# Optimization experiments

Measured on AMD Instinct MI355X. Metric: run time of the kernel, lower is better.

Reference implementation:

```python
import jax, jax.numpy as jnp
import numpy as np

SEQ = 4096
D = 1024      # input_dim
DK = 1024     # query_dim
DV = 1024     # encoding_dim
STD = 0.02


def setup_inputs() -> dict:
    key = jax.random.key(0)
    kz, kq, kk, kv = jax.random.split(key, 4)
    z = jax.random.normal(kz, (SEQ, D), dtype=jnp.float32)
    # weights stored as [in, out], matching q = z @ Wq
    Wq = STD * jax.random.normal(kq, (D, DK), dtype=jnp.float32)
    Wk = STD * jax.random.normal(kk, (D, DK), dtype=jnp.float32)
    Wv = STD * jax.random.normal(kv, (D, DV), dtype=jnp.float32)
    return {"z": z, "Wq": Wq, "Wk": Wk, "Wv": Wv}


def reference(z, Wq, Wk, Wv):
    q = z @ Wq                      # [S, dk]
    k = z @ Wk                      # [S, dk]
    v = z @ Wv                      # [S, dv]
    # NOTE: original applies the 1/sqrt(dk) scale AFTER softmax (to the probabilities)
    attn = jax.nn.softmax(q @ k.T, axis=-1) * (DK ** -0.5)  # [S, S]
    return attn @ v                 # [S, dv]
```

## Files before the change

### kernel.cpp

```cpp
#include <hip/hip_runtime.h>

typedef unsigned short u16;
typedef unsigned int u32;
typedef __attribute__((ext_vector_type(8))) short bf16x8;
typedef __attribute__((ext_vector_type(8))) _Float16 f16x8;
typedef __attribute__((ext_vector_type(4))) float f32x4;

__device__ inline u16 f2bf(float f){
  union { float f; unsigned u; } v; v.f = f;
  unsigned r = v.u + 0x7FFFu + ((v.u >> 16) & 1u);
  return (u16)(r >> 16);
}
__device__ inline float bf2f(u16 u){
  union { unsigned u; float f; } v; v.u = ((unsigned)u) << 16;
  return v.f;
}
__device__ inline u16 f2h(float f){
  union { _Float16 h; u16 u; } v; v.h = (_Float16)f; return v.u;
}

__device__ inline void gload16(const u16* g, u16* l){
  __builtin_amdgcn_global_load_lds(
      (const __attribute__((address_space(1))) u32*)(const void*)g,
      (__attribute__((address_space(3))) u32*)(void*)l, 16, 0, 0);
}

#define WAITV(n) asm volatile("s_waitcnt vmcnt(" #n ")" ::: "memory")
#define FENCE()  asm volatile("" ::: "memory")

__global__ __launch_bounds__(256) void split_f32(const float* __restrict__ x,
                                                 u16* __restrict__ hi,
                                                 u16* __restrict__ lo, int n4){
  int i = blockIdx.x * 256 + threadIdx.x;
  if (i >= n4) return;
  float4 v = ((const float4*)x)[i];
  float a0 = v.x, a1 = v.y, a2 = v.z, a3 = v.w;
  u16 h0 = f2bf(a0), h1 = f2bf(a1), h2 = f2bf(a2), h3 = f2bf(a3);
  ushort4 h; h.x = h0; h.y = h1; h.z = h2; h.w = h3;
  ushort4 l; l.x = f2bf(a0 - bf2f(h0)); l.y = f2bf(a1 - bf2f(h1));
  l.z = f2bf(a2 - bf2f(h2)); l.w = f2bf(a3 - bf2f(h3));
  ((ushort4*)hi)[i] = h;
  ((ushort4*)lo)[i] = l;
}

__global__ __launch_bounds__(256) void conv_h16(const float* __restrict__ x,
                                                u16* __restrict__ h16, int n4){
  int i = blockIdx.x * 256 + threadIdx.x;
  if (i >= n4) return;
  float4 v = ((const float4*)x)[i];
  ushort4 g; g.x = f2h(v.x); g.y = f2h(v.y); g.z = f2h(v.z); g.w = f2h(v.w);
  ((ushort4*)h16)[i] = g;
}

__global__ __launch_bounds__(256) void transpose_wv16(
    const float* __restrict__ W, u16* __restrict__ H){
  __shared__ float t[64][65];
  int d0 = blockIdx.y * 64, n0 = blockIdx.x * 64;
  int tid = threadIdx.x;
  int r = tid >> 4, c4 = (tid & 15) * 4;
  for (int rr = r; rr < 64; rr += 16){
    float4 v = *(const float4*)&W[(size_t)(d0 + rr) * 1024 + n0 + c4];
    t[rr][c4 + 0] = v.x; t[rr][c4 + 1] = v.y; t[rr][c4 + 2] = v.z; t[rr][c4 + 3] = v.w;
  }
  __syncthreads();
  int n = tid >> 4, d4 = (tid & 15) * 4;
  for (int nn = n; nn < 64; nn += 16){
    ushort4 h;
    h.x = f2h(t[d4 + 0][nn]); h.y = f2h(t[d4 + 1][nn]);
    h.z = f2h(t[d4 + 2][nn]); h.w = f2h(t[d4 + 3][nn]);
    *(ushort4*)&H[(size_t)(n0 + nn) * 1024 + d0 + d4] = h;
  }
}

template<int IN, int EPI>
__global__ __launch_bounds__(256) void gemm_bt(
    const u16* __restrict__ Ah, const u16* __restrict__ Al, int lda,
    const u16* __restrict__ Bh, const u16* __restrict__ Bl, int ldb,
    void* __restrict__ C0, int ldc, int K, size_t zslab){
  constexpr int NPL = (IN == 0) ? 4 : 2;
  constexpr int DEPTH = (IN == 0) ? 1 : 2;
  constexpr int NBUF = DEPTH + 1;
  __shared__ __align__(16) u16 sm[NBUF * NPL * 4096];

  const int kz = blockIdx.z * K;
  Ah += kz; Bh += kz;
  if constexpr (IN == 0){ Al += kz; Bl += kz; }

  const int tid = threadIdx.x;
  const int lane = tid & 63, wave = tid >> 6;
  const int wr = wave >> 1, wc = wave & 1;
  const int lr = lane & 15, kg = lane >> 4;

  const int nwg = gridDim.x * gridDim.y;
  const int id = blockIdx.y * gridDim.x + blockIdx.x;
  const int chunk = nwg >> 3;
  const int swz = (id & 7) * chunk + (id >> 3);
  const int bx = swz % gridDim.x, by = swz / gridDim.x;
  const int m0 = by * 128, n0 = bx * 128;

  const int l_r = lane >> 2, l_c = lane & 3;
  const int st_chunk = l_c ^ ((l_r + (l_r >> 2)) & 3);
  const int rd_swz = (lr + (lr >> 2)) & 3;

  f32x4 acc[4][4];
  #pragma unroll
  for (int m = 0; m < 4; m++)
    #pragma unroll
    for (int n = 0; n < 4; n++)
      acc[m][n] = (f32x4){0.f, 0.f, 0.f, 0.f};

  auto STAGE = [&](int buf, int k0){
    #pragma unroll
    for (int c = 0; c < NPL * 2; ++c){
      int pc = c * 4 + wave;
      int p = pc >> 3, ch = pc & 7;
      const u16* g; int ld, rb;
      if (IN == 0){
        g = (p == 0) ? Ah : (p == 1) ? Al : (p == 2) ? Bh : Bl;
        ld = (p < 2) ? lda : ldb;  rb = (p < 2) ? m0 : n0;
      } else {
        g = (p == 0) ? Ah : Bh;
        ld = (p == 0) ? lda : ldb; rb = (p == 0) ? m0 : n0;
      }
      int r = ch * 16 + l_r;
      const u16* src = g + (size_t)(rb + r) * ld + k0 + st_chunk * 8;
      u16* dst = &sm[((size_t)buf * NPL + p) * 4096 + ch * 512];
      gload16(src, dst);
    }
  };

  const int KT = K >> 5;
  STAGE(0, 0);
  if constexpr (DEPTH == 2){ if (KT > 1) STAGE(1, 32); }

  int bufc = 0, pfb = DEPTH % NBUF;
  for (int kt = 0; kt < KT; ++kt){
    const int pf = kt + DEPTH;
    if (pf < KT){
      STAGE(pfb, pf * 32);
      WAITV(8);
    } else if (kt + 1 < KT){
      if constexpr (IN == 0) WAITV(8); else WAITV(4);
    } else {
      WAITV(0);
    }
    __builtin_amdgcn_s_barrier();
    FENCE();

    const u16* pA  = &sm[((size_t)bufc * NPL + 0) * 4096];
    const u16* pAl = &sm[((size_t)bufc * NPL + 1) * 4096];
    const u16* pB  = &sm[((size_t)bufc * NPL + (IN == 0 ? 2 : 1)) * 4096];
    const u16* pBl = &sm[((size_t)bufc * NPL + 3) * 4096];

    const int slot = (kg ^ rd_swz) * 8;
    bf16x8 afh[4], bfh[4], afl[4], bfl[4];
    f16x8 ah16[4], bh16[4];
    #pragma unroll
    for (int m = 0; m < 4; m++){
      int r = wr * 64 + m * 16 + lr;
      if (IN == 2) ah16[m] = *(const f16x8*)&pA[r * 32 + slot];
      else {
        afh[m] = *(const bf16x8*)&pA[r * 32 + slot];
        if (IN == 0) afl[m] = *(const bf16x8*)&pAl[r * 32 + slot];
      }
    }
    #pragma unroll
    for (int n = 0; n < 4; n++){
      int r = wc * 64 + n * 16 + lr;
      if (IN == 2) bh16[n] = *(const f16x8*)&pB[r * 32 + slot];
      else {
        bfh[n] = *(const bf16x8*)&pB[r * 32 + slot];
        if (IN == 0) bfl[n] = *(const bf16x8*)&pBl[r * 32 + slot];
      }
    }
    #pragma unroll
    for (int m = 0; m < 4; m++)
      #pragma unroll
      for (int n = 0; n < 4; n++){
        if (IN == 2){
          acc[m][n] = __builtin_amdgcn_mfma_f32_16x16x32_f16(ah16[m], bh16[n], acc[m][n], 0, 0, 0);
        } else {
          acc[m][n] = __builtin_amdgcn_mfma_f32_16x16x32_bf16(afh[m], bfh[n], acc[m][n], 0, 0, 0);
          if (IN == 0){
            acc[m][n] = __builtin_amdgcn_mfma_f32_16x16x32_bf16(afl[m], bfh[n], acc[m][n], 0, 0, 0);
            acc[m][n] = __builtin_amdgcn_mfma_f32_16x16x32_bf16(afh[m], bfl[n], acc[m][n], 0, 0, 0);
          }
        }
      }
    FENCE();
    __builtin_amdgcn_s_barrier();
    bufc = (bufc + 1 == NBUF) ? 0 : bufc + 1;
    pfb  = (pfb  + 1 == NBUF) ? 0 : pfb  + 1;
  }

  const int row0 = m0 + wr * 64, col0 = n0 + wc * 64 + lr;
  #pragma unroll
  for (int m = 0; m < 4; m++)
    #pragma unroll
    for (int n = 0; n < 4; n++)
      #pragma unroll
      for (int r = 0; r < 4; r++){
        int row = row0 + m * 16 + kg * 4 + r;
        int col = col0 + n * 16;
        float x = acc[m][n][r];
        if (EPI == 0){
          float* C = (float*)C0 + (size_t)blockIdx.z * zslab;
          C[(size_t)row * ldc + col] = x;
        } else {
          ((u16*)C0)[(size_t)row * ldc + col] = f2h(x);
        }
      }
}

__global__ __launch_bounds__(512, 1) void gemm256(
    const u16* __restrict__ A, int lda,
    const u16* __restrict__ B, int ldb,
    float* __restrict__ C0z, int l0, float* __restrict__ C1z, int l1,
    float* __restrict__ C2z, int l2, float* __restrict__ C3z, int l3,
    int K){
  __shared__ __align__(16) u16 sm[2 * 32768];

  const int tid = threadIdx.x;
  const int lane = tid & 63, wave = tid >> 6;
  const int wr = wave >> 2, wc = wave & 3;
  const int lr = lane & 15, kg = lane >> 4;
  const int g7 = lr & 7;

  const int nwg = gridDim.x * gridDim.y;
  const int id = blockIdx.y * gridDim.x + blockIdx.x;
  const int chunk = nwg >> 3;
  const int swz = (id & 7) * chunk + (id >> 3);
  const int bx = swz % gridDim.x, by = swz / gridDim.x;
  const int m0 = by * 256, n0 = bx * 256;

  A += (size_t)blockIdx.z * (size_t)K;
  B += (size_t)blockIdx.z * (size_t)K;
  float* Cp; int ldc;
  if (blockIdx.z == 0){ Cp = C0z; ldc = l0; }
  else if (blockIdx.z == 1){ Cp = C1z; ldc = l1; }
  else if (blockIdx.z == 2){ Cp = C2z; ldc = l2; }
  else { Cp = C3z; ldc = l3; }

  auto STAGE = [&](int buf, int k0){
    #pragma unroll
    for (int rd = 0; rd < 8; ++rd){
      int p = rd >> 2;
      int r0 = (rd & 3) * 64 + wave * 8;
      const u16* g = p ? B : A;
      int ld = p ? ldb : lda;
      int rb = p ? n0 : m0;
      int grow = rb + r0 + (lane >> 3);
      int gch = (lane & 7) ^ (lane >> 3);
      const u16* src = g + (size_t)grow * ld + k0 + gch * 8;
      u16* dst = &sm[(size_t)buf * 32768 + p * 16384 + r0 * 64];
      gload16(src, dst);
    }
  };

  f32x4 acc[8][4];
  #pragma unroll
  for (int m = 0; m < 8; m++)
    #pragma unroll
    for (int n = 0; n < 4; n++)
      acc[m][n] = (f32x4){0.f, 0.f, 0.f, 0.f};

  const int KT = K >> 6;
  STAGE(0, 0);

  int bufc = 0;
  for (int kt = 0; kt < KT; ++kt){
    WAITV(0);
    __builtin_amdgcn_s_barrier();
    FENCE();
    if (kt + 1 < KT) STAGE(bufc ^ 1, (kt + 1) * 64);

    const u16* pA = &sm[(size_t)bufc * 32768];
    const u16* pB = pA + 16384;
    #pragma unroll
    for (int ks = 0; ks < 2; ++ks){
      f16x8 b[4], a[8];
      #pragma unroll
      for (int n = 0; n < 4; n++){
        int R = wc * 64 + n * 16 + lr;
        b[n] = *(const f16x8*)&pB[R * 64 + (((ks * 4 + kg) ^ g7) * 8)];
      }
      #pragma unroll
      for (int m = 0; m < 8; m++){
        int R = wr * 128 + m * 16 + lr;
        a[m] = *(const f16x8*)&pA[R * 64 + (((ks * 4 + kg) ^ g7) * 8)];
      }
      __builtin_amdgcn_s_setprio(1);
      #pragma unroll
      for (int m = 0; m < 8; m++)
        #pragma unroll
        for (int n = 0; n < 4; n++)
          acc[m][n] = __builtin_amdgcn_mfma_f32_16x16x32_f16(a[m], b[n], acc[m][n], 0, 0, 0);
      __builtin_amdgcn_s_setprio(0);
    }
    FENCE();
    bufc ^= 1;
  }

  const int row0 = m0 + wr * 128, col0 = n0 + wc * 64 + lr;
  #pragma unroll
  for (int m = 0; m < 8; m++)
    #pragma unroll
    for (int n = 0; n < 4; n++)
      #pragma unroll
      for (int r = 0; r < 4; r++){
        int row = row0 + m * 16 + kg * 4 + r;
        int col = col0 + n * 16;
        Cp[(size_t)row * ldc + col] = acc[m][n][r];
      }
}

__global__ __launch_bounds__(256) void reduce_t(u16* __restrict__ dst,
                                                const float* __restrict__ s0,
                                                const float* __restrict__ s1,
                                                const float* __restrict__ s2,
                                                const float* __restrict__ s3){
  int idx = blockIdx.x * 256 + threadIdx.x;
  float4 a = ((const float4*)s0)[idx];
  float4 b = ((const float4*)s1)[idx];
  float4 c = ((const float4*)s2)[idx];
  float4 d = ((const float4*)s3)[idx];
  ushort4 o;
  o.x = f2h((a.x + b.x) + (c.x + d.x));
  o.y = f2h((a.y + b.y) + (c.y + d.y));
  o.z = f2h((a.z + b.z) + (c.z + d.z));
  o.w = f2h((a.w + b.w) + (c.w + d.w));
  ((ushort4*)dst)[idx] = o;
}

__global__ __launch_bounds__(256) void reduce_pv(float* __restrict__ out,
                                                 const float* __restrict__ Sf,
                                                 const float* __restrict__ s3){
  int idx = blockIdx.x * 256 + threadIdx.x;
  int r = idx >> 8, c4 = (idx & 255) * 4;
  float4 a = ((const float4*)out)[idx];
  float4 b = ((const float4*)s3)[idx];
  float4 h1 = *(const float4*)&Sf[(size_t)r * 4096 + 2048 + c4];
  float4 h2 = *(const float4*)&Sf[(size_t)r * 4096 + 3072 + c4];
  float4 o;
  o.x = (a.x + b.x) + (h1.x + h2.x);
  o.y = (a.y + b.y) + (h1.y + h2.y);
  o.z = (a.z + b.z) + (h1.z + h2.z);
  o.w = (a.w + b.w) + (h1.w + h2.w);
  ((float4*)out)[idx] = o;
}

__global__ __launch_bounds__(256) void softmax_rows(float* __restrict__ S){
  int rrow = blockIdx.x;
  float* srow = S + (size_t)rrow * 4096;
  __shared__ float e[4096];
  __shared__ float red[4];
  int tid = threadIdx.x;

  float m = -1e30f;
  for (int i = tid * 4; i < 4096; i += 1024){
    float4 v = *(const float4*)(srow + i);
    m = fmaxf(m, fmaxf(fmaxf(v.x, v.y), fmaxf(v.z, v.w)));
  }
  for (int o = 32; o > 0; o >>= 1) m = fmaxf(m, __shfl_xor(m, o));
  if ((tid & 63) == 0) red[tid >> 6] = m;
  __syncthreads();
  m = fmaxf(fmaxf(red[0], red[1]), fmaxf(red[2], red[3]));

  float s = 0.f;
  for (int i = tid * 4; i < 4096; i += 1024){
    float4 v = *(const float4*)(srow + i);
    float4 ev;
    ev.x = __expf(v.x - m); ev.y = __expf(v.y - m);
    ev.z = __expf(v.z - m); ev.w = __expf(v.w - m);
    s += (ev.x + ev.y) + (ev.z + ev.w);
    *(float4*)&e[i] = ev;
  }
  for (int o = 32; o > 0; o >>= 1) s += __shfl_xor(s, o);
  __syncthreads();
  if ((tid & 63) == 0) red[tid >> 6] = s;
  __syncthreads();
  s = (red[0] + red[1]) + (red[2] + red[3]);

  float scale = 0.03125f / s;
  u16* prow = (u16*)((char*)S + (size_t)rrow * 16384);
  for (int i = tid * 4; i < 4096; i += 1024){
    float4 v = *(const float4*)&e[i];
    ushort4 o; o.x = f2h(v.x * scale); o.y = f2h(v.y * scale);
    o.z = f2h(v.z * scale); o.w = f2h(v.w * scale);
    *(ushort4*)(prow + i) = o;
  }
}

extern "C" void kernel_launch(void* const* d_in, const int* in_sizes, int n_in,
                              void* d_out, int out_size, void* d_ws, size_t ws_size,
                              hipStream_t stream){
  const float* z  = (const float*)d_in[0];
  const float* Wq = (const float*)d_in[1];
  const float* Wk = (const float*)d_in[2];
  const float* Wv = (const float*)d_in[3];
  char* ws = (char*)d_ws;
  const size_t MB = 1ull << 20;

  u16* t16   = (u16*)(ws + 0 * MB);
  u16* z16   = (u16*)(ws + 8 * MB);
  u16* vt16  = (u16*)(ws + 16 * MB);
  float* S   = (float*)(ws + 24 * MB);
  u16* m16   = (u16*)(ws + 88 * MB);
  float* slab3 = (float*)(ws + 0 * MB);
  u16* wqh   = (u16*)(ws + 24 * MB);
  u16* wql   = (u16*)(ws + 26 * MB);
  u16* wkh   = (u16*)(ws + 28 * MB);
  u16* wkl   = (u16*)(ws + 30 * MB);
  u16* wvt16 = (u16*)(ws + 32 * MB);
  float* msl = (float*)(ws + 40 * MB);

  conv_h16<<<4096, 256, 0, stream>>>(z, z16, 4096 * 1024 / 4);
  split_f32<<<1024, 256, 0, stream>>>(Wq, wqh, wql, 1024 * 1024 / 4);
  split_f32<<<1024, 256, 0, stream>>>(Wk, wkh, wkl, 1024 * 1024 / 4);
  transpose_wv16<<<dim3(16, 16), 256, 0, stream>>>(Wv, wvt16);

  gemm_bt<0, 0><<<dim3(8, 8, 4), 256, 0, stream>>>(wkh, wkl, 1024,
      wqh, wql, 1024, msl, 1024, 256, (size_t)1024 * 1024);
  reduce_t<<<1024, 256, 0, stream>>>(m16, msl, msl + 1048576,
      msl + 2097152, msl + 3145728);

  gemm_bt<2, 1><<<dim3(32, 8), 256, 0, stream>>>(wvt16, nullptr, 1024,
      z16, nullptr, 1024, vt16, 4096, 1024, 0);

  gemm_bt<2, 1><<<dim3(8, 32), 256, 0, stream>>>(z16, nullptr, 1024,
      m16, nullptr, 1024, t16, 1024, 1024, 0);

  gemm256<<<dim3(16, 16, 1), 512, 0, stream>>>(t16, 1024, z16, 1024,
      S, 4096, S, 4096, S, 4096, S, 4096, 1024);

  softmax_rows<<<4096, 256, 0, stream>>>(S);

  gemm256<<<dim3(4, 16, 4), 512, 0, stream>>>((u16*)S, 8192, vt16, 4096,
      (float*)d_out, 1024, S + 2048, 4096, S + 3072, 4096, slab3, 1024, 1024);

  reduce_pv<<<4096, 256, 0, stream>>>((float*)d_out, S, slab3);
}
```

Before: 176.2 us.

## Store scores in fp16, merge projection GEMMs and split kernels into single launches

The QK^T score matrix is now written as fp16 instead of fp32, which halves the score write and the softmax read traffic, and softmax works in place on fp16. The two f16 projection GEMMs (V^T and T = z·M) are merged into one 512-block launch, and the Wq/Wk split kernels are merged into one, to cut launch count and tail effects. The split-K partials of P·V now go to dedicated slabs. Rounding the logits to fp16 before softmax adds precision risk on the scores.

```diff
diff --git a/kernel.cpp b/kernel.cpp
--- a/kernel.cpp
+++ b/kernel.cpp
@@ -28,11 +28,15 @@
 #define WAITV(n) asm volatile("s_waitcnt vmcnt(" #n ")" ::: "memory")
 #define FENCE()  asm volatile("" ::: "memory")
 
-__global__ __launch_bounds__(256) void split_f32(const float* __restrict__ x,
-                                                 u16* __restrict__ hi,
-                                                 u16* __restrict__ lo, int n4){
-  int i = blockIdx.x * 256 + threadIdx.x;
-  if (i >= n4) return;
+__global__ __launch_bounds__(256) void split_wqk(const float* __restrict__ wq,
+                                                 const float* __restrict__ wk,
+                                                 u16* __restrict__ qh, u16* __restrict__ ql,
+                                                 u16* __restrict__ kh, u16* __restrict__ kl){
+  int b = blockIdx.x;
+  const float* x; u16 *hi, *lo;
+  int i;
+  if (b < 1024){ x = wq; hi = qh; lo = ql; i = b * 256 + threadIdx.x; }
+  else         { x = wk; hi = kh; lo = kl; i = (b - 1024) * 256 + threadIdx.x; }
   float4 v = ((const float4*)x)[i];
   float a0 = v.x, a1 = v.y, a2 = v.z, a3 = v.w;
   u16 h0 = f2bf(a0), h1 = f2bf(a1), h2 = f2bf(a2), h3 = f2bf(a3);
@@ -77,14 +81,13 @@
     const u16* __restrict__ Ah, const u16* __restrict__ Al, int lda,
     const u16* __restrict__ Bh, const u16* __restrict__ Bl, int ldb,
     void* __restrict__ C0, int ldc, int K, size_t zslab){
-  constexpr int NPL = (IN == 0) ? 4 : 2;
-  constexpr int DEPTH = (IN == 0) ? 1 : 2;
+  constexpr int NPL = 4;
+  constexpr int DEPTH = 1;
   constexpr int NBUF = DEPTH + 1;
   __shared__ __align__(16) u16 sm[NBUF * NPL * 4096];
 
   const int kz = blockIdx.z * K;
-  Ah += kz; Bh += kz;
-  if constexpr (IN == 0){ Al += kz; Bl += kz; }
+  Ah += kz; Bh += kz; Al += kz; Bl += kz;
 
   const int tid = threadIdx.x;
   const int lane = tid & 63, wave = tid >> 6;
@@ -114,14 +117,9 @@
     for (int c = 0; c < NPL * 2; ++c){
       int pc = c * 4 + wave;
       int p = pc >> 3, ch = pc & 7;
-      const u16* g; int ld, rb;
-      if (IN == 0){
-        g = (p == 0) ? Ah : (p == 1) ? Al : (p == 2) ? Bh : Bl;
-        ld = (p < 2) ? lda : ldb;  rb = (p < 2) ? m0 : n0;
-      } else {
-        g = (p == 0) ? Ah : Bh;
-        ld = (p == 0) ? lda : ldb; rb = (p == 0) ? m0 : n0;
-      }
+      const u16* g = (p == 0) ? Ah : (p == 1) ? Al : (p == 2) ? Bh : Bl;
+      int ld = (p < 2) ? lda : ldb;
+      int rb = (p < 2) ? m0 : n0;
       int r = ch * 16 + l_r;
       const u16* src = g + (size_t)(rb + r) * ld + k0 + st_chunk * 8;
       u16* dst = &sm[((size_t)buf * NPL + p) * 4096 + ch * 512];
@@ -131,7 +129,116 @@
 
   const int KT = K >> 5;
   STAGE(0, 0);
-  if constexpr (DEPTH == 2){ if (KT > 1) STAGE(1, 32); }
+
+  int bufc = 0, pfb = DEPTH % NBUF;
+  for (int kt = 0; kt < KT; ++kt){
+    const int pf = kt + DEPTH;
+    if (pf < KT){
+      STAGE(pfb, pf * 32);
+      WAITV(8);
+    } else {
+      WAITV(0);
+    }
+    __builtin_amdgcn_s_barrier();
+    FENCE();
+
+    const u16* pA  = &sm[((size_t)bufc * NPL + 0) * 4096];
+    const u16* pAl = &sm[((size_t)bufc * NPL + 1) * 4096];
+    const u16* pB  = &sm[((size_t)bufc * NPL + 2) * 4096];
+    const u16* pBl = &sm[((size_t)bufc * NPL + 3) * 4096];
+
+    const int slot = (kg ^ rd_swz) * 8;
+    bf16x8 afh[4], bfh[4], afl[4], bfl[4];
+    #pragma unroll
+    for (int m = 0; m < 4; m++){
+      int r = wr * 64 + m * 16 + lr;
+      afh[m] = *(const bf16x8*)&pA[r * 32 + slot];
+      afl[m] = *(const bf16x8*)&pAl[r * 32 + slot];
+    }
+    #pragma unroll
+    for (int n = 0; n < 4; n++){
+      int r = wc * 64 + n * 16 + lr;
+      bfh[n] = *(const bf16x8*)&pB[r * 32 + slot];
+      bfl[n] = *(const bf16x8*)&pBl[r * 32 + slot];
+    }
+    #pragma unroll
+    for (int m = 0; m < 4; m++)
+      #pragma unroll
+      for (int n = 0; n < 4; n++){
+        acc[m][n] = __builtin_amdgcn_mfma_f32_16x16x32_bf16(afh[m], bfh[n], acc[m][n], 0, 0, 0);
+        acc[m][n] = __builtin_amdgcn_mfma_f32_16x16x32_bf16(afl[m], bfh[n], acc[m][n], 0, 0, 0);
+        acc[m][n] = __builtin_amdgcn_mfma_f32_16x16x32_bf16(afh[m], bfl[n], acc[m][n], 0, 0, 0);
+      }
+    FENCE();
+    __builtin_amdgcn_s_barrier();
+    bufc = (bufc + 1 == NBUF) ? 0 : bufc + 1;
+    pfb  = (pfb  + 1 == NBUF) ? 0 : pfb  + 1;
+  }
+
+  const int row0 = m0 + wr * 64, col0 = n0 + wc * 64 + lr;
+  float* C = (float*)C0 + (size_t)blockIdx.z * zslab;
+  #pragma unroll
+  for (int m = 0; m < 4; m++)
+    #pragma unroll
+    for (int n = 0; n < 4; n++)
+      #pragma unroll
+      for (int r = 0; r < 4; r++){
+        int row = row0 + m * 16 + kg * 4 + r;
+        int col = col0 + n * 16;
+        C[(size_t)row * ldc + col] = acc[m][n][r];
+      }
+}
+
+__global__ __launch_bounds__(256) void gemm_dual(
+    const u16* __restrict__ A0, int lda0, const u16* __restrict__ B0, int ldb0,
+    u16* __restrict__ C0_, int ldc0, int gx0,
+    const u16* __restrict__ A1, int lda1, const u16* __restrict__ B1, int ldb1,
+    u16* __restrict__ C1_, int ldc1, int gx1, int K){
+  constexpr int NPL = 2, DEPTH = 2, NBUF = 3;
+  __shared__ __align__(16) u16 sm[NBUF * NPL * 4096];
+
+  const int id = blockIdx.x;
+  const int l = id & 255;
+  const int swz = (l & 7) * 32 + (l >> 3);
+  const u16* Ah; const u16* Bh; u16* C; int lda, ldb, ldc, gx;
+  if (id < 256){ Ah = A0; Bh = B0; C = C0_; lda = lda0; ldb = ldb0; ldc = ldc0; gx = gx0; }
+  else         { Ah = A1; Bh = B1; C = C1_; lda = lda1; ldb = ldb1; ldc = ldc1; gx = gx1; }
+  const int bx = swz % gx, by = swz / gx;
+  const int m0 = by * 128, n0 = bx * 128;
+
+  const int tid = threadIdx.x;
+  const int lane = tid & 63, wave = tid >> 6;
+  const int wr = wave >> 1, wc = wave & 1;
+  const int lr = lane & 15, kg = lane >> 4;
+  const int l_r = lane >> 2, l_c = lane & 3;
+  const int st_chunk = l_c ^ ((l_r + (l_r >> 2)) & 3);
+  const int rd_swz = (lr + (lr >> 2)) & 3;
+
+  f32x4 acc[4][4];
+  #pragma unroll
+  for (int m = 0; m < 4; m++)
+    #pragma unroll
+    for (int n = 0; n < 4; n++)
+      acc[m][n] = (f32x4){0.f, 0.f, 0.f, 0.f};
+
+  auto STAGE = [&](int buf, int k0){
+    #pragma unroll
+    for (int c = 0; c < NPL * 2; ++c){
+      int pc = c * 4 + wave;
+      int p = pc >> 3, ch = pc & 7;
+      const u16* g = (p == 0) ? Ah : Bh;
+      int ld = (p == 0) ? lda : ldb;
+      int rb = (p == 0) ? m0 : n0;
+      int r = ch * 16 + l_r;
+      const u16* src = g + (size_t)(rb + r) * ld + k0 + st_chunk * 8;
+      u16* dst = &sm[((size_t)buf * NPL + p) * 4096 + ch * 512];
+      gload16(src, dst);
+    }
+  };
+
+  const int KT = K >> 5;
+  STAGE(0, 0);
+  if (KT > 1) STAGE(1, 32);
 
   int bufc = 0, pfb = DEPTH % NBUF;
   for (int kt = 0; kt < KT; ++kt){
@@ -140,53 +247,33 @@
       STAGE(pfb, pf * 32);
       WAITV(8);
     } else if (kt + 1 < KT){
-      if constexpr (IN == 0) WAITV(8); else WAITV(4);
+      WAITV(4);
     } else {
       WAITV(0);
     }
     __builtin_amdgcn_s_barrier();
     FENCE();
 
-    const u16* pA  = &sm[((size_t)bufc * NPL + 0) * 4096];
-    const u16* pAl = &sm[((size_t)bufc * NPL + 1) * 4096];
-    const u16* pB  = &sm[((size_t)bufc * NPL + (IN == 0 ? 2 : 1)) * 4096];
-    const u16* pBl = &sm[((size_t)bufc * NPL + 3) * 4096];
+    const u16* pA = &sm[((size_t)bufc * NPL + 0) * 4096];
+    const u16* pB = &sm[((size_t)bufc * NPL + 1) * 4096];
 
     const int slot = (kg ^ rd_swz) * 8;
-    bf16x8 afh[4], bfh[4], afl[4], bfl[4];
-    f16x8 ah16[4], bh16[4];
+    f16x8 ah[4], bh[4];
     #pragma unroll
     for (int m = 0; m < 4; m++){
       int r = wr * 64 + m * 16 + lr;
-      if (IN == 2) ah16[m] = *(const f16x8*)&pA[r * 32 + slot];
-      else {
-        afh[m] = *(const bf16x8*)&pA[r * 32 + slot];
-        if (IN == 0) afl[m] = *(const bf16x8*)&pAl[r * 32 + slot];
-      }
+      ah[m] = *(const f16x8*)&pA[r * 32 + slot];
     }
     #pragma unroll
     for (int n = 0; n < 4; n++){
       int r = wc * 64 + n * 16 + lr;
-      if (IN == 2) bh16[n] = *(const f16x8*)&pB[r * 32 + slot];
-      else {
-        bfh[n] = *(const bf16x8*)&pB[r * 32 + slot];
-        if (IN == 0) bfl[n] = *(const bf16x8*)&pBl[r * 32 + slot];
-      }
+      bh[n] = *(const f16x8*)&pB[r * 32 + slot];
     }
     #pragma unroll
     for (int m = 0; m < 4; m++)
       #pragma unroll
-      for (int n = 0; n < 4; n++){
-        if (IN == 2){
-          acc[m][n] = __builtin_amdgcn_mfma_f32_16x16x32_f16(ah16[m], bh16[n], acc[m][n], 0, 0, 0);
-        } else {
-          acc[m][n] = __builtin_amdgcn_mfma_f32_16x16x32_bf16(afh[m], bfh[n], acc[m][n], 0, 0, 0);
-          if (IN == 0){
-            acc[m][n] = __builtin_amdgcn_mfma_f32_16x16x32_bf16(afl[m], bfh[n], acc[m][n], 0, 0, 0);
-            acc[m][n] = __builtin_amdgcn_mfma_f32_16x16x32_bf16(afh[m], bfl[n], acc[m][n], 0, 0, 0);
-          }
-        }
-      }
+      for (int n = 0; n < 4; n++)
+        acc[m][n] = __builtin_amdgcn_mfma_f32_16x16x32_f16(ah[m], bh[n], acc[m][n], 0, 0, 0);
     FENCE();
     __builtin_amdgcn_s_barrier();
     bufc = (bufc + 1 == NBUF) ? 0 : bufc + 1;
@@ -202,21 +289,16 @@
       for (int r = 0; r < 4; r++){
         int row = row0 + m * 16 + kg * 4 + r;
         int col = col0 + n * 16;
-        float x = acc[m][n][r];
-        if (EPI == 0){
-          float* C = (float*)C0 + (size_t)blockIdx.z * zslab;
-          C[(size_t)row * ldc + col] = x;
-        } else {
-          ((u16*)C0)[(size_t)row * ldc + col] = f2h(x);
-        }
+        C[(size_t)row * ldc + col] = f2h(acc[m][n][r]);
       }
 }
 
+template<int EPI>
 __global__ __launch_bounds__(512, 1) void gemm256(
     const u16* __restrict__ A, int lda,
     const u16* __restrict__ B, int ldb,
-    float* __restrict__ C0z, int l0, float* __restrict__ C1z, int l1,
-    float* __restrict__ C2z, int l2, float* __restrict__ C3z, int l3,
+    void* __restrict__ C0z, int l0, void* __restrict__ C1z, int l1,
+    void* __restrict__ C2z, int l2, void* __restrict__ C3z, int l3,
     int K){
   __shared__ __align__(16) u16 sm[2 * 32768];
 
@@ -235,7 +317,7 @@
 
   A += (size_t)blockIdx.z * (size_t)K;
   B += (size_t)blockIdx.z * (size_t)K;
-  float* Cp; int ldc;
+  void* Cp; int ldc;
   if (blockIdx.z == 0){ Cp = C0z; ldc = l0; }
   else if (blockIdx.z == 1){ Cp = C1z; ldc = l1; }
   else if (blockIdx.z == 2){ Cp = C2z; ldc = l2; }
@@ -310,7 +392,8 @@
       for (int r = 0; r < 4; r++){
         int row = row0 + m * 16 + kg * 4 + r;
         int col = col0 + n * 16;
-        Cp[(size_t)row * ldc + col] = acc[m][n][r];
+        if (EPI == 0) ((float*)Cp)[(size_t)row * ldc + col] = acc[m][n][r];
+        else          ((u16*)Cp)[(size_t)row * ldc + col] = f2h(acc[m][n][r]);
       }
 }
 
@@ -332,34 +415,35 @@
   ((ushort4*)dst)[idx] = o;
 }
 
-__global__ __launch_bounds__(256) void reduce_pv(float* __restrict__ out,
-                                                 const float* __restrict__ Sf,
-                                                 const float* __restrict__ s3){
+__global__ __launch_bounds__(256) void reduce_pv4(float* __restrict__ out,
+                                                  const float* __restrict__ s1,
+                                                  const float* __restrict__ s2,
+                                                  const float* __restrict__ s3){
   int idx = blockIdx.x * 256 + threadIdx.x;
-  int r = idx >> 8, c4 = (idx & 255) * 4;
   float4 a = ((const float4*)out)[idx];
-  float4 b = ((const float4*)s3)[idx];
-  float4 h1 = *(const float4*)&Sf[(size_t)r * 4096 + 2048 + c4];
-  float4 h2 = *(const float4*)&Sf[(size_t)r * 4096 + 3072 + c4];
+  float4 b = ((const float4*)s1)[idx];
+  float4 c = ((const float4*)s2)[idx];
+  float4 d = ((const float4*)s3)[idx];
   float4 o;
-  o.x = (a.x + b.x) + (h1.x + h2.x);
-  o.y = (a.y + b.y) + (h1.y + h2.y);
-  o.z = (a.z + b.z) + (h1.z + h2.z);
-  o.w = (a.w + b.w) + (h1.w + h2.w);
+  o.x = (a.x + b.x) + (c.x + d.x);
+  o.y = (a.y + b.y) + (c.y + d.y);
+  o.z = (a.z + b.z) + (c.z + d.z);
+  o.w = (a.w + b.w) + (c.w + d.w);
   ((float4*)out)[idx] = o;
 }
 
-__global__ __launch_bounds__(256) void softmax_rows(float* __restrict__ S){
-  int rrow = blockIdx.x;
-  float* srow = S + (size_t)rrow * 4096;
+__global__ __launch_bounds__(256) void softmax16(u16* __restrict__ S){
+  int row = blockIdx.x;
+  _Float16* srow = (_Float16*)(S + (size_t)row * 4096);
   __shared__ float e[4096];
   __shared__ float red[4];
   int tid = threadIdx.x;
 
   float m = -1e30f;
-  for (int i = tid * 4; i < 4096; i += 1024){
-    float4 v = *(const float4*)(srow + i);
-    m = fmaxf(m, fmaxf(fmaxf(v.x, v.y), fmaxf(v.z, v.w)));
+  for (int i = tid * 8; i < 4096; i += 2048){
+    f16x8 v = *(const f16x8*)(srow + i);
+    #pragma unroll
+    for (int j = 0; j < 8; j++) m = fmaxf(m, (float)v[j]);
   }
   for (int o = 32; o > 0; o >>= 1) m = fmaxf(m, __shfl_xor(m, o));
   if ((tid & 63) == 0) red[tid >> 6] = m;
@@ -367,13 +451,14 @@
   m = fmaxf(fmaxf(red[0], red[1]), fmaxf(red[2], red[3]));
 
   float s = 0.f;
-  for (int i = tid * 4; i < 4096; i += 1024){
-    float4 v = *(const float4*)(srow + i);
-    float4 ev;
-    ev.x = __expf(v.x - m); ev.y = __expf(v.y - m);
-    ev.z = __expf(v.z - m); ev.w = __expf(v.w - m);
-    s += (ev.x + ev.y) + (ev.z + ev.w);
-    *(float4*)&e[i] = ev;
+  for (int i = tid * 8; i < 4096; i += 2048){
+    f16x8 v = *(const f16x8*)(srow + i);
+    #pragma unroll
+    for (int j = 0; j < 8; j++){
+      float ev = __expf((float)v[j] - m);
+      s += ev;
+      e[i + j] = ev;
+    }
   }
   for (int o = 32; o > 0; o >>= 1) s += __shfl_xor(s, o);
   __syncthreads();
@@ -382,12 +467,11 @@
   s = (red[0] + red[1]) + (red[2] + red[3]);
 
   float scale = 0.03125f / s;
-  u16* prow = (u16*)((char*)S + (size_t)rrow * 16384);
-  for (int i = tid * 4; i < 4096; i += 1024){
-    float4 v = *(const float4*)&e[i];
-    ushort4 o; o.x = f2h(v.x * scale); o.y = f2h(v.y * scale);
-    o.z = f2h(v.z * scale); o.w = f2h(v.w * scale);
-    *(ushort4*)(prow + i) = o;
+  for (int i = tid * 8; i < 4096; i += 2048){
+    f16x8 o;
+    #pragma unroll
+    for (int j = 0; j < 8; j++) o[j] = (_Float16)(e[i + j] * scale);
+    *(f16x8*)(srow + i) = o;
   }
 }
 
@@ -404,9 +488,11 @@
   u16* t16   = (u16*)(ws + 0 * MB);
   u16* z16   = (u16*)(ws + 8 * MB);
   u16* vt16  = (u16*)(ws + 16 * MB);
-  float* S   = (float*)(ws + 24 * MB);
+  u16* S16   = (u16*)(ws + 24 * MB);
   u16* m16   = (u16*)(ws + 88 * MB);
-  float* slab3 = (float*)(ws + 0 * MB);
+  float* pv1 = (float*)(ws + 56 * MB);
+  float* pv2 = (float*)(ws + 72 * MB);
+  float* pv3 = (float*)(ws + 0 * MB);
   u16* wqh   = (u16*)(ws + 24 * MB);
   u16* wql   = (u16*)(ws + 26 * MB);
   u16* wkh   = (u16*)(ws + 28 * MB);
@@ -415,8 +501,7 @@
   float* msl = (float*)(ws + 40 * MB);
 
   conv_h16<<<4096, 256, 0, stream>>>(z, z16, 4096 * 1024 / 4);
-  split_f32<<<1024, 256, 0, stream>>>(Wq, wqh, wql, 1024 * 1024 / 4);
-  split_f32<<<1024, 256, 0, stream>>>(Wk, wkh, wkl, 1024 * 1024 / 4);
+  split_wqk<<<2048, 256, 0, stream>>>(Wq, Wk, wqh, wql, wkh, wkl);
   transpose_wv16<<<dim3(16, 16), 256, 0, stream>>>(Wv, wvt16);
 
   gemm_bt<0, 0><<<dim3(8, 8, 4), 256, 0, stream>>>(wkh, wkl, 1024,
@@ -424,19 +509,17 @@
   reduce_t<<<1024, 256, 0, stream>>>(m16, msl, msl + 1048576,
       msl + 2097152, msl + 3145728);
 
-  gemm_bt<2, 1><<<dim3(32, 8), 256, 0, stream>>>(wvt16, nullptr, 1024,
-      z16, nullptr, 1024, vt16, 4096, 1024, 0);
-
-  gemm_bt<2, 1><<<dim3(8, 32), 256, 0, stream>>>(z16, nullptr, 1024,
-      m16, nullptr, 1024, t16, 1024, 1024, 0);
-
-  gemm256<<<dim3(16, 16, 1), 512, 0, stream>>>(t16, 1024, z16, 1024,
-      S, 4096, S, 4096, S, 4096, S, 4096, 1024);
-
-  softmax_rows<<<4096, 256, 0, stream>>>(S);
-
-  gemm256<<<dim3(4, 16, 4), 512, 0, stream>>>((u16*)S, 8192, vt16, 4096,
-      (float*)d_out, 1024, S + 2048, 4096, S + 3072, 4096, slab3, 1024, 1024);
-
-  reduce_pv<<<4096, 256, 0, stream>>>((float*)d_out, S, slab3);
-}
+  gemm_dual<<<512, 256, 0, stream>>>(
+      z16, 1024, m16, 1024, t16, 1024, 8,
+      wvt16, 1024, z16, 1024, vt16, 4096, 32, 1024);
+
+  gemm256<1><<<dim3(16, 16, 1), 512, 0, stream>>>(t16, 1024, z16, 1024,
+      S16, 4096, S16, 4096, S16, 4096, S16, 4096, 1024);
+
+  softmax16<<<4096, 256, 0, stream>>>(S16);
+
+  gemm256<0><<<dim3(4, 16, 4), 512, 0, stream>>>(S16, 4096, vt16, 4096,
+      (float*)d_out, 1024, pv1, 1024, pv2, 1024, pv3, 1024, 1024);
+
+  reduce_pv4<<<4096, 256, 0, stream>>>((float*)d_out, pv1, pv2, pv3);
+}
```

Result: faster. 158.5 us, median of 2 (-10.0%).
